# Kernel tuning notes

Measured on AMD Instinct MI355X. Metric: run time of the kernel, lower is better.

The kernel has to match this reference:

```python
import jax, jax.numpy as jnp
import numpy as np

N, C, T, V, O, S, R = 32, 64, 256, 25, 192, 3, 8  # batch, in_ch, time, joints, out_ch, subsets, rel_ch


def setup_inputs() -> dict:
    key = jax.random.key(0)
    ks = jax.random.split(key, 20)
    w = lambda i, shape: (jax.random.normal(ks[i], shape, jnp.float32) * 0.05)
    return {
        "x": jax.random.normal(ks[0], (N, C, T, V), jnp.float32),
        "spd_A": jax.random.normal(ks[1], (V, V), jnp.float32) * 0.1,
        "A3": jax.random.normal(ks[2], (S, V, V), jnp.float32) * 0.1,
        "A6": jax.random.normal(ks[3], (6, V, V), jnp.float32) * 0.1,
        "conv1_w": w(4, (S, R, C)), "conv1_b": jnp.zeros((S, R), jnp.float32),
        "conv2_w": w(5, (S, R, C)), "conv2_b": jnp.zeros((S, R), jnp.float32),
        "conv4_w": w(6, (S, O, R)), "conv4_b": jnp.zeros((S, O), jnp.float32),
        "conv3_w": w(7, (S, O, C)), "conv3_b": jnp.zeros((S, O), jnp.float32),
        "alpha": jnp.full((1,), 0.5, jnp.float32),
        "beta": jnp.full((1,), 0.5, jnp.float32),
        "gamma": jnp.full((1,), 0.5, jnp.float32),
        "bn_w": jnp.ones((O,), jnp.float32), "bn_b": jnp.zeros((O,), jnp.float32),
        "down_w": w(8, (O, C)), "down_b": jnp.zeros((O,), jnp.float32),
        "dbn_w": jnp.ones((O,), jnp.float32), "dbn_b": jnp.zeros((O,), jnp.float32),
    }


def _bn(y, w, b):
    # BatchNorm2d in training mode: stats over (N, T, V) per channel, biased var
    mu = y.mean(axis=(0, 2, 3), keepdims=True)
    var = ((y - mu) ** 2).mean(axis=(0, 2, 3), keepdims=True)
    return (y - mu) * jax.lax.rsqrt(var + 1e-5) * w[None, :, None, None] + b[None, :, None, None]


def reference(x, spd_A, A3, A6, conv1_w, conv1_b, conv2_w, conv2_b, conv4_w, conv4_b,
              conv3_w, conv3_b, alpha, beta, gamma, bn_w, bn_b, down_w, down_b, dbn_w, dbn_b):
    out_c = conv4_w.shape[1]
    # A6 expanded: (out//6, 6, V, V) -> (out, V, V); contiguous-view == tile along channel blocks
    A6_ex = jnp.tile(A6, (out_c // 6, 1, 1))  # (O, V, V)
    # 1x1 conv then temporal mean == conv on temporal mean (linear op commutes)
    xm = x.mean(axis=2)  # (N, C, V)
    x1 = jnp.einsum('ncv,src->nsrv', xm, conv1_w) + conv1_b[None, :, :, None]
    x2 = jnp.einsum('ncv,src->nsrv', xm, conv2_w) + conv2_b[None, :, :, None]
    d = jnp.tanh(x1[..., :, None] - x2[..., None, :])  # (N, S, R, V, V)
    A_dyn = jnp.einsum('nsruv,sor->nsouv', d, conv4_w) + conv4_b[None, :, :, None, None]
    A_at = (A_dyn * alpha + A3[None, :, None, :, :]
            + A6_ex[None, None] * beta + spd_A[None, None, None] * gamma)  # (N, S, O, V, V)
    # CTRGC_2: x3 = conv3(x); einsum 'ncuv,nctv->nctu', summed over subsets
    x3 = jnp.einsum('nctv,soc->nsotv', x, conv3_w) + conv3_b[None, :, :, None, None]
    y = jnp.einsum('nsouv,nsotv->notu', A_at, x3)  # (N, O, T, V)
    y = _bn(y, bn_w, bn_b)
    xd = jnp.einsum('nctv,oc->notv', x, down_w) + down_b[None, :, None, None]
    y = jax.nn.relu(y + _bn(xd, dbn_w, dbn_b))
    return y
```

## Files before the change

### kernel.cpp

```cpp
#include <hip/hip_runtime.h>

#define N_ 32
#define C_ 64
#define T_ 256
#define V_ 25
#define O_ 192
#define S_ 3
#define R_ 8
#define VV (V_*V_)
#define TV (T_*V_)
#define RP 26
#define TRP (T_*RP)

typedef unsigned short u16;
typedef unsigned int u32;
typedef __attribute__((ext_vector_type(4))) u16 u16x4;
typedef __attribute__((ext_vector_type(8))) u16 u16x8;
typedef __attribute__((ext_vector_type(4))) u32 u32x4;
typedef __attribute__((ext_vector_type(8))) __bf16 bf16x8;
typedef __attribute__((ext_vector_type(4))) float f32x4;

#define WS_A2F_U 0
#define WS_XQ_U  (18874368)
#define WS_XD_U  (18874368 + 13631488)
#define WS_YB_U  (18874368 + 13631488 + 39321600)
#define WS_XM_F   (55574528)
#define WS_RS_F   (55574528 + 51200)
#define WS_STAT_F (55574528 + 51200 + 153600)
#define WS_COEF_F (55574528 + 51200 + 153600 + 768)

__device__ __forceinline__ u16 f2b(float f) {
    return __builtin_bit_cast(u16, (__bf16)f);
}
__device__ __forceinline__ float b2f(u16 u) {
    return __builtin_bit_cast(float, ((unsigned)u) << 16);
}
__device__ __forceinline__ f32x4 mfma16(bf16x8 a, bf16x8 b, f32x4 c) {
    return __builtin_amdgcn_mfma_f32_16x16x32_bf16(a, b, c, 0, 0, 0);
}

__global__ void k0_xq(const float* __restrict__ x, u16* __restrict__ xq,
                      float* __restrict__ xm) {
    __shared__ float tile[64][52];
    int bid = blockIdx.x;
    int n = bid >> 7, tb = bid & 127;
    int t0 = tb * 2;
    int tid = threadIdx.x;
    const float2* xp = (const float2*)(x + (size_t)n * C_ * TV + t0 * 25);
    for (int p = tid; p < 1600; p += 256) {
        int c = p / 25, q = p % 25;
        float2 f2 = xp[(size_t)c * 3200 + q];
        tile[c][q * 2] = f2.x;
        tile[c][q * 2 + 1] = f2.y;
    }
    __syncthreads();
    for (int p = tid; p < 832; p += 256) {
        int row = p >> 4, c4g = p & 15;
        int t = row >= RP, v = row - t * RP;
        u16x4 w;
        #pragma unroll
        for (int i = 0; i < 4; ++i) {
            int co = ((c4g & 3) << 4) + ((c4g >> 2) << 2) + i;
            w[i] = (v < 25) ? f2b(tile[co][t * 25 + v]) : (u16)0;
        }
        *(u16x4*)&xq[((size_t)n * TRP + tb * 52 + row) * 64 + c4g * 4] = w;
    }
    for (int p = tid; p < 1600; p += 256) {
        int c = p / 25, v = p % 25;
        float s = (tile[c][v] + tile[c][25 + v]) * (1.f / T_);
        atomicAdd(&xm[((size_t)n * C_ + c) * V_ + v], s);
    }
}

__global__ void k2_a2f(const float* __restrict__ spd, const float* __restrict__ A3,
                       const float* __restrict__ A6,
                       const float* __restrict__ w1, const float* __restrict__ b1,
                       const float* __restrict__ w2, const float* __restrict__ b2,
                       const float* __restrict__ w4, const float* __restrict__ b4,
                       const float* __restrict__ b3,
                       const float* __restrict__ alpha, const float* __restrict__ beta,
                       const float* __restrict__ gamma,
                       u16* __restrict__ a2f, const float* __restrict__ xmbuf,
                       float* __restrict__ rs_tot) {
    __shared__ float xm[C_ * V_];
    __shared__ float x1s[R_ * V_], x2s[R_ * V_];
    __shared__ float dm[R_ * VV];
    __shared__ float a3s[VV], sps[VV], a6s[6 * VV];
    __shared__ float aat[2 * VV];
    __shared__ float w4s[2][R_];
    __shared__ float b4s[2];
    int bid = blockIdx.x;
    int n = bid / 24;
    int rem = bid % 24;
    int s = rem / 8, og = rem % 8;
    int tid = threadIdx.x;
    const float* xmg = xmbuf + (size_t)n * C_ * V_;
    for (int p = tid; p < C_ * V_; p += 256) xm[p] = xmg[p];
    for (int p = tid; p < VV; p += 256) { a3s[p] = A3[s * VV + p]; sps[p] = spd[p]; }
    for (int p = tid; p < 6 * VV; p += 256) a6s[p] = A6[p];
    __syncthreads();
    if (tid < R_ * V_) {
        int r = tid / V_, v = tid % V_;
        float acc1 = b1[s * R_ + r], acc2 = b2[s * R_ + r];
        for (int c = 0; c < C_; ++c) {
            float xv = xm[c * V_ + v];
            acc1 += xv * w1[(s * R_ + r) * C_ + c];
            acc2 += xv * w2[(s * R_ + r) * C_ + c];
        }
        x1s[tid] = acc1; x2s[tid] = acc2;
    }
    __syncthreads();
    for (int p = tid; p < R_ * VV; p += 256) {
        int r = p / VV, uv = p % VV, u = uv / V_, v = uv % V_;
        dm[p] = tanhf(x1s[r * V_ + u] - x2s[r * V_ + v]);
    }
    __syncthreads();
    float al = alpha[0], be = beta[0], ga = gamma[0];
    for (int op = 0; op < 12; ++op) {
        int o0 = og * 24 + op * 2;
        if (tid < 16) w4s[tid >> 3][tid & 7] =
            w4[((size_t)(s * O_ + o0 + (tid >> 3))) * R_ + (tid & 7)];
        if (tid < 2) b4s[tid] = b4[s * O_ + o0 + tid];
        __syncthreads();
        for (int p = tid; p < 2 * VV; p += 256) {
            int oo = p / VV, pp = p % VV;
            float acc = b4s[oo];
            #pragma unroll
            for (int r = 0; r < R_; ++r) acc += dm[r * VV + pp] * w4s[oo][r];
            int o = o0 + oo;
            aat[p] = al * acc + a3s[pp] + be * a6s[(o % 6) * VV + pp] + ga * sps[pp];
        }
        __syncthreads();
        if (tid < 2 * V_) {
            int oo = tid / V_, u = tid % V_;
            float rs = 0.f;
            for (int v = 0; v < V_; ++v) rs += aat[oo * VV + u * V_ + v];
            atomicAdd(&rs_tot[((size_t)(n * O_ + o0 + oo)) * V_ + u],
                      b3[s * O_ + o0 + oo] * rs);
        }
        {
            int oo = tid >> 7, l2 = tid & 127, cu = l2 >> 6, l = l2 & 63;
            int u = cu * 16 + (l & 15);
            u16x8 w;
            #pragma unroll
            for (int j = 0; j < 8; ++j) {
                int v = ((j >> 2) << 4) + ((l >> 4) << 2) + (j & 3);
                float val = 0.f;
                if (u < V_ && v < V_) val = aat[oo * VV + u * V_ + v];
                w[j] = f2b(val);
            }
            size_t idx = ((((size_t)(n * O_ + o0 + oo)) * S_ + s) * 2 + cu) * 64 + l;
            ((u16x8*)a2f)[idx] = w;
        }
        __syncthreads();
    }
}

#define OSTR_B 2504
#define SSTR_B 832
#define BUF_B  20064

__global__ __launch_bounds__(256, 3)
void k3_main(const u16* __restrict__ xq,
             const float* __restrict__ w3, const float* __restrict__ dw,
             const float* __restrict__ db,
             const u16* __restrict__ a2f, const float* __restrict__ rs_tot,
             u16* __restrict__ yb16, u16* __restrict__ xdws,
             float* __restrict__ stats) {
    __shared__ char x3Lb[2 * BUF_B];
    __shared__ u16 xdst[8 * 416];
    __shared__ u16 ystage[8 * 400];
    int orig = blockIdx.x;
    int bid = (orig & 7) * 96 + (orig >> 3);
    int n = bid / 24;
    int o0 = (bid % 24) * 8;
    int tid = threadIdx.x, wid = tid >> 6, lane = tid & 63;
    int lr = lane & 15, lg = lane >> 4;
    int colt = wid & 1;
    int rt0 = (wid >> 1) * 13;

    for (int p = tid; p < 2 * BUF_B / 16; p += 256) ((u32x4*)x3Lb)[p] = u32x4{0,0,0,0};

    const float* wsrc = (colt == 0)
        ? w3 + ((size_t)((lr >> 3) * O_ + o0 + (lr & 7))) * C_
        : ((lr < 8) ? w3 + ((size_t)(2 * O_ + o0 + lr)) * C_
                    : dw + ((size_t)(o0 + lr - 8)) * C_);
    bf16x8 bw[2];
    #pragma unroll
    for (int ks = 0; ks < 2; ++ks) {
        u16x8 tmp;
        #pragma unroll
        for (int j = 0; j < 8; ++j) {
            int c = ks * 32 + (lg << 2) + (j & 3) + ((j >> 2) << 4);
            tmp[j] = f2b(wsrc[c]);
        }
        bw[ks] = __builtin_bit_cast(bf16x8, tmp);
    }
    float dbv = (colt == 1 && lr >= 8) ? db[o0 + lr - 8] : 0.f;

    int wo = (colt == 0) ? (lr & 7) : lr;
    int wsb = (colt == 0) ? (lr >> 3) : 2;
    int colbyte = wo * OSTR_B + wsb * SSTR_B;

    const bf16x8* a2v = (const bf16x8*)a2f;
    bf16x8 Bh[2][6];
    float rsb0[2], rsb1[2];
    #pragma unroll
    for (int oi = 0; oi < 2; ++oi) {
        int o = o0 + (wid << 1) + oi;
        const bf16x8* bp = a2v + ((size_t)(n * O_ + o)) * 6 * 64 + lane;
        #pragma unroll
        for (int q = 0; q < 6; ++q) Bh[oi][q] = bp[(size_t)q * 64];
        const float* rsp = rs_tot + ((size_t)(n * O_ + o)) * V_;
        rsb0[oi] = rsp[lr];
        rsb1[oi] = (lr < 9) ? rsp[16 + lr] : 0.f;
    }

    float sy1[2] = {0, 0}, sy2[2] = {0, 0};
    float sd1 = 0.f, sd2 = 0.f;
    const u16* xbn = xq + (size_t)n * TRP * 64;
    int rdw = 13 * lr + 2 * lg;
    __syncthreads();

    for (int ch = 0; ch < 16; ++ch) {
        int t0 = ch * 16;
        char* buf = x3Lb + (ch & 1) * BUF_B;
        const u16* xrow = xbn + (size_t)t0 * RP * 64;
        for (int rt = rt0; rt < rt0 + 13; ++rt) {
            const u16* ap = xrow + (size_t)(rt * 16 + lr) * 64 + (lg << 4);
            u16x8 A0 = *(const u16x8*)ap;
            u16x8 A1 = *(const u16x8*)(ap + 8);
            f32x4 acc = {0.f, 0.f, 0.f, 0.f};
            acc = mfma16(__builtin_bit_cast(bf16x8, A0), bw[0], acc);
            acc = mfma16(__builtin_bit_cast(bf16x8, A1), bw[1], acc);
            int rbase = rt * 16 + (lg << 2);
            if (colt == 0 || lr < 8) {
                u16x4 w;
                #pragma unroll
                for (int reg = 0; reg < 4; ++reg) w[reg] = f2b(acc[reg]);
                *(u16x4*)(buf + colbyte + rbase * 2) = w;
            } else {
                u16x4 w;
                #pragma unroll
                for (int reg = 0; reg < 4; ++reg) {
                    int rr = rbase + reg;
                    int t = rr / RP, v = rr - t * RP;
                    float val = acc[reg] + dbv;
                    w[reg] = f2b(val);
                    if (v < 25) { sd1 += val; sd2 += val * val; }
                }
                *(u16x4*)&xdst[(lr - 8) * 416 + rbase] = w;
            }
        }
        __syncthreads();
        #pragma unroll
        for (int oi = 0; oi < 2; ++oi) {
            int ol = (wid << 1) + oi;
            const u32* L = (const u32*)(buf + ol * OSTR_B);
            f32x4 acc0 = {0, 0, 0, 0}, acc1 = {0, 0, 0, 0};
            #pragma unroll
            for (int s = 0; s < 3; ++s) {
                const u32* Ls = L + s * 208 + rdw;
                u32 d0 = Ls[0], d1 = Ls[1], d8 = Ls[8], d9 = Ls[9];
                bf16x8 A = __builtin_bit_cast(bf16x8, u32x4{d0, d1, d8, d9});
                acc0 = mfma16(A, Bh[oi][s * 2 + 0], acc0);
                acc1 = mfma16(A, Bh[oi][s * 2 + 1], acc1);
            }
            int ylb = ol * 400 + (lg << 2) * 25;
            #pragma unroll
            for (int reg = 0; reg < 4; ++reg) {
                float v0 = acc0[reg] + rsb0[oi];
                ystage[ylb + reg * 25 + lr] = f2b(v0);
                sy1[oi] += v0; sy2[oi] += v0 * v0;
                if (lr < 9) {
                    float v1 = acc1[reg] + rsb1[oi];
                    ystage[ylb + reg * 25 + 16 + lr] = f2b(v1);
                    sy1[oi] += v1; sy2[oi] += v1 * v1;
                }
            }
        }
        {
            size_t ygb = (size_t)(n * O_ + o0) * TV + (size_t)t0 * V_;
            for (int q = lane; q < 100; q += 64) {
                int sel = q >= 50;
                int ol2 = (wid << 1) + sel;
                int j = q - sel * 50;
                u16x8 pk = *(const u16x8*)&ystage[ol2 * 400 + j * 8];
                *(u16x8*)&yb16[ygb + (size_t)ol2 * TV + j * 8] = pk;
            }
        }
        if (colt == 1) {
            int tofs = (wid >> 1) * 8;
            size_t gdb = (size_t)(n * O_ + o0) * TV + (size_t)(t0 + tofs) * V_;
            for (int q = lane; q < 200; q += 64) {
                int o = q / 25, w = q - o * 25;
                int g0 = w * 8;
                int tl = g0 / 25, v = g0 - tl * 25;
                u16x8 pk;
                #pragma unroll
                for (int k = 0; k < 8; ++k) {
                    pk[k] = xdst[o * 416 + (tofs + tl) * RP + v];
                    if (++v == 25) { v = 0; ++tl; }
                }
                *(u16x8*)&xdws[gdb + (size_t)o * TV + g0] = pk;
            }
        }
    }
    #pragma unroll
    for (int oi = 0; oi < 2; ++oi) {
        float v1 = sy1[oi], v2 = sy2[oi];
        #pragma unroll
        for (int m = 1; m < 64; m <<= 1) {
            v1 += __shfl_xor(v1, m);
            v2 += __shfl_xor(v2, m);
        }
        if (lane == 0) {
            atomicAdd(&stats[0 * O_ + o0 + (wid << 1) + oi], v1);
            atomicAdd(&stats[1 * O_ + o0 + (wid << 1) + oi], v2);
        }
    }
    if (colt == 1) {
        float v1 = sd1, v2 = sd2;
        v1 += __shfl_xor(v1, 16); v2 += __shfl_xor(v2, 16);
        v1 += __shfl_xor(v1, 32); v2 += __shfl_xor(v2, 32);
        if (lane >= 8 && lane < 16) {
            atomicAdd(&stats[2 * O_ + o0 + lane - 8], v1);
            atomicAdd(&stats[3 * O_ + o0 + lane - 8], v2);
        }
    }
}

__global__ void k4_coef(const float* __restrict__ bn_w, const float* __restrict__ bn_b,
                        const float* __restrict__ dbn_w, const float* __restrict__ dbn_b,
                        const float* __restrict__ stats, float* __restrict__ coef) {
    int o = threadIdx.x;
    if (o >= O_) return;
    float inv = 1.f / (float)(N_ * T_ * V_);
    float mu_y = stats[o] * inv;
    float var_y = stats[O_ + o] * inv - mu_y * mu_y;
    float ay = bn_w[o] * rsqrtf(var_y + 1e-5f);
    float by = bn_b[o] - mu_y * ay;
    float mu_d = stats[2 * O_ + o] * inv;
    float var_d = stats[3 * O_ + o] * inv - mu_d * mu_d;
    float ad = dbn_w[o] * rsqrtf(var_d + 1e-5f);
    float bd = dbn_b[o] - mu_d * ad;
    coef[o] = ay; coef[O_ + o] = by; coef[2 * O_ + o] = ad; coef[3 * O_ + o] = bd;
}

__global__ void k5_final(float* __restrict__ out, const u16* __restrict__ yb,
                         const u16* __restrict__ xd, const float* __restrict__ cf) {
    size_t total = (size_t)N_ * O_ * TV / 8;
    for (size_t i = blockIdx.x * (size_t)blockDim.x + threadIdx.x; i < total;
         i += (size_t)gridDim.x * blockDim.x) {
        int o = (int)((i / 800) % O_);
        float ay = cf[o], by = cf[O_ + o], ad = cf[2 * O_ + o], bd = cf[3 * O_ + o];
        u16x8 yv = ((const u16x8*)yb)[i];
        u16x8 dv = ((const u16x8*)xd)[i];
        float4 r0, r1;
        r0.x = fmaxf(ay * b2f(yv[0]) + by + ad * b2f(dv[0]) + bd, 0.f);
        r0.y = fmaxf(ay * b2f(yv[1]) + by + ad * b2f(dv[1]) + bd, 0.f);
        r0.z = fmaxf(ay * b2f(yv[2]) + by + ad * b2f(dv[2]) + bd, 0.f);
        r0.w = fmaxf(ay * b2f(yv[3]) + by + ad * b2f(dv[3]) + bd, 0.f);
        r1.x = fmaxf(ay * b2f(yv[4]) + by + ad * b2f(dv[4]) + bd, 0.f);
        r1.y = fmaxf(ay * b2f(yv[5]) + by + ad * b2f(dv[5]) + bd, 0.f);
        r1.z = fmaxf(ay * b2f(yv[6]) + by + ad * b2f(dv[6]) + bd, 0.f);
        r1.w = fmaxf(ay * b2f(yv[7]) + by + ad * b2f(dv[7]) + bd, 0.f);
        ((float4*)out)[2 * i] = r0;
        ((float4*)out)[2 * i + 1] = r1;
    }
}

extern "C" void kernel_launch(void* const* d_in, const int* in_sizes, int n_in,
                              void* d_out, int out_size, void* d_ws, size_t ws_size,
                              hipStream_t stream) {
    const float* x     = (const float*)d_in[0];
    const float* spd   = (const float*)d_in[1];
    const float* A3    = (const float*)d_in[2];
    const float* A6    = (const float*)d_in[3];
    const float* w1    = (const float*)d_in[4];
    const float* b1    = (const float*)d_in[5];
    const float* w2    = (const float*)d_in[6];
    const float* b2    = (const float*)d_in[7];
    const float* w4    = (const float*)d_in[8];
    const float* b4    = (const float*)d_in[9];
    const float* w3    = (const float*)d_in[10];
    const float* b3    = (const float*)d_in[11];
    const float* alpha = (const float*)d_in[12];
    const float* beta  = (const float*)d_in[13];
    const float* gamma = (const float*)d_in[14];
    const float* bn_w  = (const float*)d_in[15];
    const float* bn_b  = (const float*)d_in[16];
    const float* dw    = (const float*)d_in[17];
    const float* db    = (const float*)d_in[18];
    const float* dbn_w = (const float*)d_in[19];
    const float* dbn_b = (const float*)d_in[20];
    float* out = (float*)d_out;
    u16*   wsu = (u16*)d_ws;
    float* wsf = (float*)d_ws;

    u16* a2f  = wsu + WS_A2F_U;
    u16* xq   = wsu + WS_XQ_U;
    u16* xd   = wsu + WS_XD_U;
    u16* yb   = wsu + WS_YB_U;
    float* xm    = wsf + WS_XM_F;
    float* rs    = wsf + WS_RS_F;
    float* stats = wsf + WS_STAT_F;
    float* coef  = wsf + WS_COEF_F;

    hipMemsetAsync(xm, 0, (N_ * C_ * V_ + N_ * O_ * V_ + 4 * O_) * sizeof(float),
                   stream);

    k0_xq<<<N_ * 128, 256, 0, stream>>>(x, xq, xm);
    k2_a2f<<<N_ * S_ * 8, 256, 0, stream>>>(spd, A3, A6, w1, b1, w2, b2, w4, b4, b3,
                                            alpha, beta, gamma, a2f, xm, rs);
    k3_main<<<N_ * 24, 256, 0, stream>>>(xq, w3, dw, db, a2f, rs, yb, xd, stats);
    k4_coef<<<1, 256, 0, stream>>>(bn_w, bn_b, dbn_w, dbn_b, stats, coef);
    k5_final<<<4096, 256, 0, stream>>>(out, yb, xd, coef);
}
```

Baseline: 335.3 us.

## Replace xm atomics with separate reduction kernel and prefetch next chunk tiles in main loop

The temporal mean xm is no longer built with per-block float atomicAdds in k0. A new k1_xm kernel now reduces the bf16 xq buffer over time for each (n, v) and writes it directly, which also shrinks the memset. In k3_main, the first four row tiles of the next time chunk are loaded before the barrier so global load latency overlaps the MFMA work. The mean is now taken from bf16-rounded inputs, a small precision change, and the extra launch plus the prefetch registers add cost.

```diff
diff --git a/kernel.cpp b/kernel.cpp
--- a/kernel.cpp
+++ b/kernel.cpp
@@ -39,8 +39,7 @@
     return __builtin_amdgcn_mfma_f32_16x16x32_bf16(a, b, c, 0, 0, 0);
 }
 
-__global__ void k0_xq(const float* __restrict__ x, u16* __restrict__ xq,
-                      float* __restrict__ xm) {
+__global__ void k0_xq(const float* __restrict__ x, u16* __restrict__ xq) {
     __shared__ float tile[64][52];
     int bid = blockIdx.x;
     int n = bid >> 7, tb = bid & 127;
@@ -65,10 +64,27 @@
         }
         *(u16x4*)&xq[((size_t)n * TRP + tb * 52 + row) * 64 + c4g * 4] = w;
     }
-    for (int p = tid; p < 1600; p += 256) {
-        int c = p / 25, v = p % 25;
-        float s = (tile[c][v] + tile[c][25 + v]) * (1.f / T_);
-        atomicAdd(&xm[((size_t)n * C_ + c) * V_ + v], s);
+}
+
+__global__ void k1_xm(const u16* __restrict__ xq, float* __restrict__ xm_out) {
+    __shared__ float ps[256];
+    int bid = blockIdx.x;
+    int n = bid / 25, v = bid % 25;
+    int tid = threadIdx.x;
+    int cg = tid & 63, tg = tid >> 6;
+    const u16* p = xq + (size_t)n * TRP * 64 + ((size_t)(tg * 64 * RP + v)) * 64 + cg;
+    float s = 0.f;
+    for (int t = 0; t < 64; ++t) {
+        s += b2f(*p);
+        p += RP * 64;
+    }
+    ps[tid] = s;
+    __syncthreads();
+    if (tid < 64) {
+        float tot = ps[tid] + ps[64 + tid] + ps[128 + tid] + ps[192 + tid];
+        int c4g = tid >> 2, i = tid & 3;
+        int co = ((c4g & 3) << 4) + ((c4g >> 2) << 2) + i;
+        xm_out[((size_t)n * C_ + co) * V_ + v] = tot * (1.f / T_);
     }
 }
 
@@ -220,37 +236,59 @@
     float sd1 = 0.f, sd2 = 0.f;
     const u16* xbn = xq + (size_t)n * TRP * 64;
     int rdw = 13 * lr + 2 * lg;
-    __syncthreads();
+    char* buf = x3Lb;
+    int t0 = 0;
+
+    auto tl = [&](int ch, int j, u16x8& A0, u16x8& A1) {
+        const u16* p = xbn + ((size_t)(ch * 16) * RP + (size_t)((rt0 + j) * 16 + lr)) * 64
+                       + (lg << 4);
+        A0 = *(const u16x8*)p;
+        A1 = *(const u16x8*)(p + 8);
+    };
+    auto proc = [&](int rt, u16x8 A0, u16x8 A1) {
+        f32x4 acc = {0.f, 0.f, 0.f, 0.f};
+        acc = mfma16(__builtin_bit_cast(bf16x8, A0), bw[0], acc);
+        acc = mfma16(__builtin_bit_cast(bf16x8, A1), bw[1], acc);
+        int rbase = rt * 16 + (lg << 2);
+        if (colt == 0 || lr < 8) {
+            u16x4 w;
+            #pragma unroll
+            for (int reg = 0; reg < 4; ++reg) w[reg] = f2b(acc[reg]);
+            *(u16x4*)(buf + colbyte + rbase * 2) = w;
+        } else {
+            u16x4 w;
+            #pragma unroll
+            for (int reg = 0; reg < 4; ++reg) {
+                int rr = rbase + reg;
+                int t = rr / RP, v = rr - t * RP;
+                float val = acc[reg] + dbv;
+                w[reg] = f2b(val);
+                if (v < 25) { sd1 += val; sd2 += val * val; }
+            }
+            *(u16x4*)&xdst[(lr - 8) * 416 + rbase] = w;
+        }
+    };
+
+    __syncthreads();
+
+    u16x8 p0a, p0b, p1a, p1b, p2a, p2b, p3a, p3b;
+    tl(0, 0, p0a, p0b); tl(0, 1, p1a, p1b); tl(0, 2, p2a, p2b); tl(0, 3, p3a, p3b);
 
     for (int ch = 0; ch < 16; ++ch) {
-        int t0 = ch * 16;
-        char* buf = x3Lb + (ch & 1) * BUF_B;
-        const u16* xrow = xbn + (size_t)t0 * RP * 64;
-        for (int rt = rt0; rt < rt0 + 13; ++rt) {
-            const u16* ap = xrow + (size_t)(rt * 16 + lr) * 64 + (lg << 4);
-            u16x8 A0 = *(const u16x8*)ap;
-            u16x8 A1 = *(const u16x8*)(ap + 8);
-            f32x4 acc = {0.f, 0.f, 0.f, 0.f};
-            acc = mfma16(__builtin_bit_cast(bf16x8, A0), bw[0], acc);
-            acc = mfma16(__builtin_bit_cast(bf16x8, A1), bw[1], acc);
-            int rbase = rt * 16 + (lg << 2);
-            if (colt == 0 || lr < 8) {
-                u16x4 w;
-                #pragma unroll
-                for (int reg = 0; reg < 4; ++reg) w[reg] = f2b(acc[reg]);
-                *(u16x4*)(buf + colbyte + rbase * 2) = w;
-            } else {
-                u16x4 w;
-                #pragma unroll
-                for (int reg = 0; reg < 4; ++reg) {
-                    int rr = rbase + reg;
-                    int t = rr / RP, v = rr - t * RP;
-                    float val = acc[reg] + dbv;
-                    w[reg] = f2b(val);
-                    if (v < 25) { sd1 += val; sd2 += val * val; }
-                }
-                *(u16x4*)&xdst[(lr - 8) * 416 + rbase] = w;
-            }
+        t0 = ch * 16;
+        buf = x3Lb + (ch & 1) * BUF_B;
+        proc(rt0 + 0, p0a, p0b);
+        proc(rt0 + 1, p1a, p1b);
+        proc(rt0 + 2, p2a, p2b);
+        proc(rt0 + 3, p3a, p3b);
+        for (int j = 4; j < 13; ++j) {
+            u16x8 A0, A1;
+            tl(ch, j, A0, A1);
+            proc(rt0 + j, A0, A1);
+        }
+        if (ch < 15) {
+            tl(ch + 1, 0, p0a, p0b); tl(ch + 1, 1, p1a, p1b);
+            tl(ch + 1, 2, p2a, p2b); tl(ch + 1, 3, p3a, p3b);
         }
         __syncthreads();
         #pragma unroll
@@ -295,12 +333,12 @@
             for (int q = lane; q < 200; q += 64) {
                 int o = q / 25, w = q - o * 25;
                 int g0 = w * 8;
-                int tl = g0 / 25, v = g0 - tl * 25;
+                int tl2 = g0 / 25, v = g0 - tl2 * 25;
                 u16x8 pk;
                 #pragma unroll
                 for (int k = 0; k < 8; ++k) {
-                    pk[k] = xdst[o * 416 + (tofs + tl) * RP + v];
-                    if (++v == 25) { v = 0; ++tl; }
+                    pk[k] = xdst[o * 416 + (tofs + tl2) * RP + v];
+                    if (++v == 25) { v = 0; ++tl2; }
                 }
                 *(u16x8*)&xdws[gdb + (size_t)o * TV + g0] = pk;
             }
@@ -407,10 +445,10 @@
     float* stats = wsf + WS_STAT_F;
     float* coef  = wsf + WS_COEF_F;
 
-    hipMemsetAsync(xm, 0, (N_ * C_ * V_ + N_ * O_ * V_ + 4 * O_) * sizeof(float),
-                   stream);
-
-    k0_xq<<<N_ * 128, 256, 0, stream>>>(x, xq, xm);
+    hipMemsetAsync(rs, 0, (N_ * O_ * V_ + 4 * O_) * sizeof(float), stream);
+
+    k0_xq<<<N_ * 128, 256, 0, stream>>>(x, xq);
+    k1_xm<<<N_ * 25, 256, 0, stream>>>(xq, xm);
     k2_a2f<<<N_ * S_ * 8, 256, 0, stream>>>(spd, A3, A6, w1, b1, w2, b2, w4, b4, b3,
                                             alpha, beta, gamma, a2f, xm, rs);
     k3_main<<<N_ * 24, 256, 0, stream>>>(xq, w3, dw, db, a2f, rs, yb, xd, stats);
```

Result: faster. 315.4 us (-5.9%).
